# Performance work log

Measured on AMD Instinct MI355X. Metric: run time of the kernel, lower is better.

Reference implementation:

```python
import jax, jax.numpy as jnp
import numpy as np

THRESH = 0.7  # similarity_threshold from __init__
EPS = 1e-8    # torch cosine_similarity eps


def setup_inputs() -> dict:
    key = jax.random.key(0)
    ks = jax.random.split(key, 7)
    B, D, F, H, M, NMEM = 65536, 512, 10, 512, 256, 1024
    return {
        "query_features": jax.random.normal(ks[0], (B, D), jnp.float32),
        "B_mat": jax.random.normal(ks[1], (D, F), jnp.float32),
        "W1": jax.random.normal(ks[2], (2 * F, H), jnp.float32) * 0.05,
        "b1": jax.random.normal(ks[3], (H,), jnp.float32) * 0.01,
        "W2": jax.random.normal(ks[4], (H, M), jnp.float32) * 0.05,
        "b2": jax.random.normal(ks[5], (M,), jnp.float32) * 0.01,
        "memory_bank": jax.random.normal(ks[6], (NMEM, M), jnp.float32),
    }


def reference(query_features, B_mat, W1, b1, W2, b2, memory_bank):
    # Fourier features (eq. 8): [B, 2F]
    xp = query_features @ B_mat
    ff = jnp.concatenate([jnp.sin(xp), jnp.cos(xp)], axis=-1)
    # memory_net MLP -> query vectors [B, M]
    h = jax.nn.relu(ff @ W1 + b1)
    q = h @ W2 + b2
    # cosine similarity q vs memory bank (torch semantics: dot / max(|a||b|, eps))
    qn = jnp.linalg.norm(q, axis=-1, keepdims=True)          # [B,1]
    mn = jnp.linalg.norm(memory_bank, axis=-1, keepdims=True)  # [N,1]
    sim = (q @ memory_bank.T) / jnp.maximum(qn * mn.T, EPS)   # [B,N]
    max_sim = jnp.max(sim, axis=1)                            # [B]
    max_idx = jnp.argmax(sim, axis=1)                         # [B]
    relevant = memory_bank[max_idx]                           # [B,M] gather
    relevant = jnp.where((max_sim < THRESH)[:, None], 0.0, relevant)
    return relevant
```

## Files before the change

kernel.cpp:

```cpp
#include <hip/hip_runtime.h>
#include <hip/hip_bf16.h>


typedef __attribute__((ext_vector_type(8))) short short8;
typedef __attribute__((ext_vector_type(4))) float f32x4;

#define MFMA(a, b, c) __builtin_amdgcn_mfma_f32_16x16x32_bf16((a), (b), (c), 0, 0, 0)

static __device__ __forceinline__ short bfb(float f) {
  return (short)__builtin_bit_cast(unsigned short, __float2bfloat16(f));
}
static __device__ __forceinline__ unsigned short bf16bits(float f) {
  return __builtin_bit_cast(unsigned short, __float2bfloat16(f));
}
static __device__ __forceinline__ float sel10(const float a[10], int i) {
  float v = a[0];
#pragma unroll
  for (int j = 1; j < 10; ++j) v = (i == j) ? a[j] : v;
  return v;
}

typedef const __attribute__((address_space(1))) unsigned int* gas_p;
typedef __attribute__((address_space(3))) unsigned int* las_p;
static __device__ __forceinline__ void async16(const void* g, void* l) {
  __builtin_amdgcn_global_load_lds((gas_p)g, (las_p)l, 16, 0, 0);
}

__global__ __launch_bounds__(256) void prep_ff_kernel(
    const float* __restrict__ W1, const float* __restrict__ W2,
    const float* __restrict__ mem, const float* __restrict__ query,
    const float* __restrict__ Bmat, __hip_bfloat16* __restrict__ W1p,
    __hip_bfloat16* __restrict__ W2p, __hip_bfloat16* __restrict__ Mp,
    __hip_bfloat16* __restrict__ ff) {
  __shared__ __align__(16) float Bl[10 * 512];
  const int b = blockIdx.x, tid = threadIdx.x;
  if (b < 16) {
    float* invl = Bl;
    const int w = tid >> 6, lane = tid & 63, g = lane >> 4, jj = lane & 15;
    {
      int r = w * 16 + jj;
      const float4* m4 = (const float4*)(mem + (size_t)(b * 64 + r) * 256);
      float ss = 0.f;
      for (int t = 0; t < 16; ++t) {
        float4 v = m4[g * 16 + t];
        ss += v.x * v.x + v.y * v.y + v.z * v.z + v.w * v.w;
      }
      ss += __shfl_xor(ss, 16);
      ss += __shfl_xor(ss, 32);
      if (g == 0) invl[r] = rsqrtf(fmaxf(ss, 1e-30f));
    }
    __syncthreads();
    for (int u = 0; u < 64; ++u) {
      int t = u * 256 + tid;
      int j = t & 7, lane2 = (t >> 3) & 63, kt = (t >> 9) & 7, nl = t >> 12;
      int g2 = lane2 >> 4, jp = lane2 & 15;
      int nloc = nl * 16 + jp;
      int kap = 32 * kt + 16 * (j >> 2) + 4 * g2 + (j & 3);
      float v = mem[(size_t)(b * 64 + nloc) * 256 + kap] * invl[nloc];
      Mp[(size_t)b * 16384 + t] = __float2bfloat16(v);
    }
  } else if (b == 16) {
    for (int idx = tid; idx < 16384; idx += 256) {
      int j = idx & 7, lane2 = (idx >> 3) & 63, ct = idx >> 9;
      int g2 = lane2 >> 4, jp = lane2 & 15;
      int k = 8 * g2 + j;
      float v = (k < 20) ? W1[k * 512 + ct * 16 + jp] : 0.f;
      W1p[idx] = __float2bfloat16(v);
    }
  } else if (b < 33) {
    int bb = b - 17;
    for (int u = 0; u < 32; ++u) {
      int idx = bb * 8192 + u * 256 + tid;
      int j = idx & 7, lane2 = (idx >> 3) & 63, c = (idx >> 9) & 15, kt = idx >> 13;
      int g2 = lane2 >> 4, jp = lane2 & 15;
      int kap = 32 * kt + 16 * (j >> 2) + 4 * g2 + (j & 3);
      W2p[idx] = __float2bfloat16(W2[(size_t)kap * 256 + c * 16 + jp]);
    }
  } else {
    const int bb = b - 33;
    for (int i = tid; i < 5120; i += 256) {
      int d = i / 10, f = i - d * 10;
      Bl[f * 512 + d] = Bmat[i];
    }
    __syncthreads();
    const int wv = tid >> 6, lane = tid & 63;
    const int g = lane >> 4, jj = lane & 15;
    const long r0 = (long)bb * 32 + (wv * 4 + g) * 2;
    const float4* qa = (const float4*)(query + r0 * 512);
    const float4* qb = (const float4*)(query + (r0 + 1) * 512);

    float acc[2][10];
#pragma unroll
    for (int f = 0; f < 10; ++f) { acc[0][f] = 0.f; acc[1][f] = 0.f; }
#pragma unroll
    for (int k = 0; k < 8; ++k) {
      float4 va = qa[jj + 16 * k];
      float4 vb = qb[jj + 16 * k];
#pragma unroll
      for (int f = 0; f < 10; ++f) {
        float4 bv = *(const float4*)(Bl + f * 512 + 4 * (jj + 16 * k));
        acc[0][f] = fmaf(va.x, bv.x, fmaf(va.y, bv.y, fmaf(va.z, bv.z, fmaf(va.w, bv.w, acc[0][f]))));
        acc[1][f] = fmaf(vb.x, bv.x, fmaf(vb.y, bv.y, fmaf(vb.z, bv.z, fmaf(vb.w, bv.w, acc[1][f]))));
      }
    }
#pragma unroll
    for (int r = 0; r < 2; ++r) {
#pragma unroll
      for (int f = 0; f < 10; ++f) {
        float s = acc[r][f];
        s += __shfl_xor(s, 1); s += __shfl_xor(s, 2);
        s += __shfl_xor(s, 4); s += __shfl_xor(s, 8);
        acc[r][f] = s;
      }
      int base = (jj < 5) ? 2 * jj : 2 * jj - 10;
      float a0 = sel10(acc[r], base);
      float a1 = sel10(acc[r], base + 1);
      float v0 = 0.f, v1 = 0.f;
      if (jj < 5) { v0 = sinf(a0); v1 = sinf(a1); }
      else if (jj < 10) { v0 = cosf(a0); v1 = cosf(a1); }
      ushort2 pk;
      pk.x = bf16bits(v0);
      pk.y = bf16bits(v1);
      ((ushort2*)ff)[(r0 + r) * 16 + jj] = pk;
    }
  }
}

#define STAGE_W2(slab, bufi)                                      \
  do {                                                            \
    const char* s_ = (const char*)W2p + (slab)*16384 + tid * 16;  \
    char* d_ = lds + (bufi)*16384 + tid * 16;                     \
    async16(s_, d_);                                              \
    async16(s_ + 4096, d_ + 4096);                                \
    async16(s_ + 8192, d_ + 8192);                                \
    async16(s_ + 12288, d_ + 12288);                              \
  } while (0)

#define STAGE_MP(slab, bufi)                                      \
  do {                                                            \
    const char* s_ = (const char*)Mp + (slab)*16384 + tid * 16;   \
    char* d_ = lds + 32768 + (bufi)*16384 + tid * 16;             \
    async16(s_, d_);                                              \
    async16(s_ + 4096, d_ + 4096);                                \
    async16(s_ + 8192, d_ + 8192);                                \
    async16(s_ + 12288, d_ + 12288);                              \
  } while (0)

__global__ __launch_bounds__(256, 2) void mega_kernel(
    const __hip_bfloat16* __restrict__ ff, const __hip_bfloat16* __restrict__ W1p,
    const float* __restrict__ b1, const __hip_bfloat16* __restrict__ W2p,
    const float* __restrict__ b2, const __hip_bfloat16* __restrict__ Mp,
    const float* __restrict__ mem, float* __restrict__ out) {
  __shared__ __align__(16) char lds[65536];
  const int tid = threadIdx.x, w = tid >> 6, lane = tid & 63;
  const int g = lane >> 4, jj = lane & 15;
  const int rowBase = blockIdx.x * 128 + w * 32;
  const f32x4 z4 = {0.f, 0.f, 0.f, 0.f};
  const short8* w1f = (const short8*)W1p;

  STAGE_W2(0, 0);

  short8 ffq[2];
#pragma unroll
  for (int rt = 0; rt < 2; ++rt)
    ffq[rt] = *(const short8*)(ff + (size_t)(rowBase + rt * 16 + jj) * 32 + g * 8);

  f32x4 acc3[2][16];
#pragma unroll
  for (int rt = 0; rt < 2; ++rt)
#pragma unroll
    for (int c = 0; c < 16; ++c) acc3[rt][c] = z4;

  short8 w1c0 = w1f[lane], w1c1 = w1f[64 + lane];

  __syncthreads();

  for (int t = 0; t < 16; ++t) {
    if (t < 15) STAGE_W2(t + 1, (t + 1) & 1);
    else STAGE_MP(0, 0);
    short8 w1n0 = w1c0, w1n1 = w1c1;
    if (t < 15) {
      w1n0 = w1f[(2 * t + 2) * 64 + lane];
      w1n1 = w1f[(2 * t + 3) * 64 + lane];
    }
    const char* buf = lds + (t & 1) * 16384;
    short8 hf[2];
#pragma unroll
    for (int half = 0; half < 2; ++half) {
      const int ct = 2 * t + half;
      f32x4 bb = *(const f32x4*)(b1 + ct * 16 + 4 * g);
      short8 a = half ? w1c1 : w1c0;
#pragma unroll
      for (int rt = 0; rt < 2; ++rt) {
        f32x4 d = MFMA(a, ffq[rt], z4);
#pragma unroll
        for (int i = 0; i < 4; ++i) {
          float v = d[i] + bb[i];
          v = v > 0.f ? v : 0.f;
          hf[rt][half * 4 + i] = bfb(v);
        }
      }
    }
#pragma unroll
    for (int c = 0; c < 16; ++c) {
      short8 bfr = *(const short8*)(buf + c * 1024 + lane * 16);
#pragma unroll
      for (int rt = 0; rt < 2; ++rt)
        acc3[rt][c] = MFMA(bfr, hf[rt], acc3[rt][c]);
    }
    w1c0 = w1n0;
    w1c1 = w1n1;
    __syncthreads();
  }

  short8 qfrag[2][8];
  float invqn[2];
#pragma unroll
  for (int rt = 0; rt < 2; ++rt) {
    float qn = 0.f;
#pragma unroll
    for (int c = 0; c < 16; ++c) {
      f32x4 bb = *(const f32x4*)(b2 + c * 16 + 4 * g);
#pragma unroll
      for (int i = 0; i < 4; ++i) {
        float v = acc3[rt][c][i] + bb[i];
        qn += v * v;
        qfrag[rt][c >> 1][(c & 1) * 4 + i] = bfb(v);
      }
    }
    qn += __shfl_xor(qn, 16);
    qn += __shfl_xor(qn, 32);
    invqn[rt] = rsqrtf(fmaxf(qn, 1e-30f));
  }

  float runmax[2][4];
  int runidx[2][4];
#pragma unroll
  for (int rt = 0; rt < 2; ++rt)
#pragma unroll
    for (int i = 0; i < 4; ++i) { runmax[rt][i] = -1e30f; runidx[rt][i] = 0; }

  for (int t = 0; t < 32; ++t) {
    if (t < 31) STAGE_MP(t + 1, (t + 1) & 1);
    const char* buf = lds + 32768 + (t & 1) * 16384;
    f32x4 a4[2][2];
#pragma unroll
    for (int rt = 0; rt < 2; ++rt)
#pragma unroll
      for (int nl = 0; nl < 2; ++nl) a4[rt][nl] = z4;
#pragma unroll
    for (int kt = 0; kt < 8; ++kt) {
#pragma unroll
      for (int nl = 0; nl < 2; ++nl) {
        short8 bfr = *(const short8*)(buf + (nl * 8 + kt) * 1024 + lane * 16);
#pragma unroll
        for (int rt = 0; rt < 2; ++rt)
          a4[rt][nl] = MFMA(qfrag[rt][kt], bfr, a4[rt][nl]);
      }
    }
#pragma unroll
    for (int nl = 0; nl < 2; ++nl) {
      int n = (t * 2 + nl) * 16 + jj;
#pragma unroll
      for (int rt = 0; rt < 2; ++rt)
#pragma unroll
        for (int i = 0; i < 4; ++i) {
          if (a4[rt][nl][i] > runmax[rt][i]) {
            runmax[rt][i] = a4[rt][nl][i];
            runidx[rt][i] = n;
          }
        }
    }
    __syncthreads();
  }

  const float4* mem4 = (const float4*)mem;
  float4* out4 = (float4*)out;
#pragma unroll
  for (int rt = 0; rt < 2; ++rt) {
#pragma unroll
    for (int i = 0; i < 4; ++i) {
#pragma unroll
      for (int o = 1; o < 16; o <<= 1) {
        float v2 = __shfl_xor(runmax[rt][i], o);
        int i2 = __shfl_xor(runidx[rt][i], o);
        if (v2 > runmax[rt][i] || (v2 == runmax[rt][i] && i2 < runidx[rt][i])) {
          runmax[rt][i] = v2;
          runidx[rt][i] = i2;
        }
      }
    }
#pragma unroll
    for (int i = 0; i < 4; ++i) {
      float iq = __shfl(invqn[rt], 4 * g + i, 64);
      float ms = runmax[rt][i] * iq;
      int s = (ms < 0.7f) ? -1 : runidx[rt][i];
      size_t row = (size_t)rowBase + rt * 16 + 4 * g + i;
#pragma unroll
      for (int cq = 0; cq < 4; ++cq) {
        int col = cq * 16 + jj;
        float4 v = {0.f, 0.f, 0.f, 0.f};
        if (s >= 0) v = mem4[(size_t)s * 64 + col];
        out4[row * 64 + col] = v;
      }
    }
  }
}

extern "C" void kernel_launch(void* const* d_in, const int* in_sizes, int n_in,
                              void* d_out, int out_size, void* d_ws, size_t ws_size,
                              hipStream_t stream) {
  const float* query = (const float*)d_in[0];
  const float* Bmat = (const float*)d_in[1];
  const float* W1 = (const float*)d_in[2];
  const float* b1 = (const float*)d_in[3];
  const float* W2 = (const float*)d_in[4];
  const float* b2 = (const float*)d_in[5];
  const float* mem = (const float*)d_in[6];
  float* out = (float*)d_out;

  char* ws = (char*)d_ws;
  __hip_bfloat16* ff = (__hip_bfloat16*)ws;
  __hip_bfloat16* Mp = (__hip_bfloat16*)(ws + 4194304);
  __hip_bfloat16* W2p = (__hip_bfloat16*)(ws + 4194304 + 524288);
  __hip_bfloat16* W1p = (__hip_bfloat16*)(ws + 4194304 + 786432);

  prep_ff_kernel<<<dim3(2081), dim3(256), 0, stream>>>(W1, W2, mem, query, Bmat,
                                                       W1p, W2p, Mp, ff);
  mega_kernel<<<dim3(512), dim3(256), 0, stream>>>(ff, W1p, b1, W2p, b2, Mp, mem, out);
}
```

Baseline: 101.0 us.

## Unify W2 and memory-bank staging into a triple-buffered 8KB slab pipeline

```diff
diff --git a/kernel.cpp b/kernel.cpp
--- a/kernel.cpp
+++ b/kernel.cpp
@@ -27,11 +27,11 @@
 }
 
 __global__ __launch_bounds__(256) void prep_ff_kernel(
-    const float* __restrict__ W1, const float* __restrict__ W2,
-    const float* __restrict__ mem, const float* __restrict__ query,
-    const float* __restrict__ Bmat, __hip_bfloat16* __restrict__ W1p,
-    __hip_bfloat16* __restrict__ W2p, __hip_bfloat16* __restrict__ Mp,
-    __hip_bfloat16* __restrict__ ff) {
+    const float* __restrict__ W1, const float* __restrict__ b1,
+    const float* __restrict__ W2, const float* __restrict__ mem,
+    const float* __restrict__ query, const float* __restrict__ Bmat,
+    __hip_bfloat16* __restrict__ W1p, __hip_bfloat16* __restrict__ W2p,
+    __hip_bfloat16* __restrict__ Mp, __hip_bfloat16* __restrict__ ff) {
   __shared__ __align__(16) float Bl[10 * 512];
   const int b = blockIdx.x, tid = threadIdx.x;
   if (b < 16) {
@@ -64,7 +64,9 @@
       int j = idx & 7, lane2 = (idx >> 3) & 63, ct = idx >> 9;
       int g2 = lane2 >> 4, jp = lane2 & 15;
       int k = 8 * g2 + j;
-      float v = (k < 20) ? W1[k * 512 + ct * 16 + jp] : 0.f;
+      float v = 0.f;
+      if (k < 20) v = W1[k * 512 + ct * 16 + jp];
+      else if (k == 20) v = b1[ct * 16 + jp];
       W1p[idx] = __float2bfloat16(v);
     }
   } else if (b < 33) {
@@ -118,6 +120,7 @@
       float v0 = 0.f, v1 = 0.f;
       if (jj < 5) { v0 = sinf(a0); v1 = sinf(a1); }
       else if (jj < 10) { v0 = cosf(a0); v1 = cosf(a1); }
+      else if (jj == 10) { v0 = 1.0f; }
       ushort2 pk;
       pk.x = bf16bits(v0);
       pk.y = bf16bits(v1);
@@ -126,113 +129,44 @@
   }
 }
 
-#define STAGE_W2(slab, bufi)                                      \
-  do {                                                            \
-    const char* s_ = (const char*)W2p + (slab)*16384 + tid * 16;  \
-    char* d_ = lds + (bufi)*16384 + tid * 16;                     \
-    async16(s_, d_);                                              \
-    async16(s_ + 4096, d_ + 4096);                                \
-    async16(s_ + 8192, d_ + 8192);                                \
-    async16(s_ + 12288, d_ + 12288);                              \
-  } while (0)
-
-#define STAGE_MP(slab, bufi)                                      \
-  do {                                                            \
-    const char* s_ = (const char*)Mp + (slab)*16384 + tid * 16;   \
-    char* d_ = lds + 32768 + (bufi)*16384 + tid * 16;             \
-    async16(s_, d_);                                              \
-    async16(s_ + 4096, d_ + 4096);                                \
-    async16(s_ + 8192, d_ + 8192);                                \
-    async16(s_ + 12288, d_ + 12288);                              \
+#define STAGE_SLAB(s)                                                       \
+  do {                                                                      \
+    const char* s_ = ((s) < 32 ? (const char*)W2p + (size_t)(s) * 8192      \
+                               : (const char*)Mp + (size_t)((s) - 32) * 8192); \
+    char* d_ = lds + 33792 + ((s) % 3) * 8192;                              \
+    async16(s_ + tid * 16, d_ + tid * 16);                                  \
+    async16(s_ + 4096 + tid * 16, d_ + 4096 + tid * 16);                    \
   } while (0)
 
 __global__ __launch_bounds__(256, 2) void mega_kernel(
     const __hip_bfloat16* __restrict__ ff, const __hip_bfloat16* __restrict__ W1p,
-    const float* __restrict__ b1, const __hip_bfloat16* __restrict__ W2p,
-    const float* __restrict__ b2, const __hip_bfloat16* __restrict__ Mp,
-    const float* __restrict__ mem, float* __restrict__ out) {
-  __shared__ __align__(16) char lds[65536];
+    const __hip_bfloat16* __restrict__ W2p, const float* __restrict__ b2,
+    const __hip_bfloat16* __restrict__ Mp, const float* __restrict__ mem,
+    float* __restrict__ out) {
+  __shared__ __align__(16) char lds[58368];
   const int tid = threadIdx.x, w = tid >> 6, lane = tid & 63;
   const int g = lane >> 4, jj = lane & 15;
   const int rowBase = blockIdx.x * 128 + w * 32;
   const f32x4 z4 = {0.f, 0.f, 0.f, 0.f};
-  const short8* w1f = (const short8*)W1p;
-
-  STAGE_W2(0, 0);
-
-  short8 ffq[2];
-#pragma unroll
-  for (int rt = 0; rt < 2; ++rt)
-    ffq[rt] = *(const short8*)(ff + (size_t)(rowBase + rt * 16 + jj) * 32 + g * 8);
+
+  short8 ffq0 = *(const short8*)(ff + (size_t)(rowBase + jj) * 32 + g * 8);
+  short8 ffq1 = *(const short8*)(ff + (size_t)(rowBase + 16 + jj) * 32 + g * 8);
+  {
+    float v = b2[tid];
+    *(float*)(lds + 32768 + tid * 4) = v;
+  }
+#pragma unroll
+  for (int r = 0; r < 8; ++r)
+    async16((const char*)W1p + r * 4096 + tid * 16, lds + r * 4096 + tid * 16);
+  STAGE_SLAB(0);
+  STAGE_SLAB(1);
 
   f32x4 acc3[2][16];
 #pragma unroll
-  for (int rt = 0; rt < 2; ++rt)
-#pragma unroll
-    for (int c = 0; c < 16; ++c) acc3[rt][c] = z4;
-
-  short8 w1c0 = w1f[lane], w1c1 = w1f[64 + lane];
-
-  __syncthreads();
-
-  for (int t = 0; t < 16; ++t) {
-    if (t < 15) STAGE_W2(t + 1, (t + 1) & 1);
-    else STAGE_MP(0, 0);
-    short8 w1n0 = w1c0, w1n1 = w1c1;
-    if (t < 15) {
-      w1n0 = w1f[(2 * t + 2) * 64 + lane];
-      w1n1 = w1f[(2 * t + 3) * 64 + lane];
-    }
-    const char* buf = lds + (t & 1) * 16384;
-    short8 hf[2];
-#pragma unroll
-    for (int half = 0; half < 2; ++half) {
-      const int ct = 2 * t + half;
-      f32x4 bb = *(const f32x4*)(b1 + ct * 16 + 4 * g);
-      short8 a = half ? w1c1 : w1c0;
-#pragma unroll
-      for (int rt = 0; rt < 2; ++rt) {
-        f32x4 d = MFMA(a, ffq[rt], z4);
-#pragma unroll
-        for (int i = 0; i < 4; ++i) {
-          float v = d[i] + bb[i];
-          v = v > 0.f ? v : 0.f;
-          hf[rt][half * 4 + i] = bfb(v);
-        }
-      }
-    }
-#pragma unroll
-    for (int c = 0; c < 16; ++c) {
-      short8 bfr = *(const short8*)(buf + c * 1024 + lane * 16);
-#pragma unroll
-      for (int rt = 0; rt < 2; ++rt)
-        acc3[rt][c] = MFMA(bfr, hf[rt], acc3[rt][c]);
-    }
-    w1c0 = w1n0;
-    w1c1 = w1n1;
-    __syncthreads();
-  }
-
+  for (int c = 0; c < 16; ++c) { acc3[0][c] = z4; acc3[1][c] = z4; }
+  short8 hf0, hf1;
   short8 qfrag[2][8];
   float invqn[2];
-#pragma unroll
-  for (int rt = 0; rt < 2; ++rt) {
-    float qn = 0.f;
-#pragma unroll
-    for (int c = 0; c < 16; ++c) {
-      f32x4 bb = *(const f32x4*)(b2 + c * 16 + 4 * g);
-#pragma unroll
-      for (int i = 0; i < 4; ++i) {
-        float v = acc3[rt][c][i] + bb[i];
-        qn += v * v;
-        qfrag[rt][c >> 1][(c & 1) * 4 + i] = bfb(v);
-      }
-    }
-    qn += __shfl_xor(qn, 16);
-    qn += __shfl_xor(qn, 32);
-    invqn[rt] = rsqrtf(fmaxf(qn, 1e-30f));
-  }
-
   float runmax[2][4];
   int runidx[2][4];
 #pragma unroll
@@ -240,38 +174,83 @@
 #pragma unroll
     for (int i = 0; i < 4; ++i) { runmax[rt][i] = -1e30f; runidx[rt][i] = 0; }
 
-  for (int t = 0; t < 32; ++t) {
-    if (t < 31) STAGE_MP(t + 1, (t + 1) & 1);
-    const char* buf = lds + 32768 + (t & 1) * 16384;
-    f32x4 a4[2][2];
-#pragma unroll
-    for (int rt = 0; rt < 2; ++rt)
-#pragma unroll
-      for (int nl = 0; nl < 2; ++nl) a4[rt][nl] = z4;
-#pragma unroll
-    for (int kt = 0; kt < 8; ++kt) {
-#pragma unroll
-      for (int nl = 0; nl < 2; ++nl) {
-        short8 bfr = *(const short8*)(buf + (nl * 8 + kt) * 1024 + lane * 16);
-#pragma unroll
-        for (int rt = 0; rt < 2; ++rt)
-          a4[rt][nl] = MFMA(qfrag[rt][kt], bfr, a4[rt][nl]);
-      }
-    }
-#pragma unroll
-    for (int nl = 0; nl < 2; ++nl) {
-      int n = (t * 2 + nl) * 16 + jj;
-#pragma unroll
-      for (int rt = 0; rt < 2; ++rt)
+  for (int t = 0; t < 96; ++t) {
+    if (t < 95) {
+      asm volatile("s_waitcnt vmcnt(2)" ::: "memory");
+    } else {
+      asm volatile("s_waitcnt vmcnt(0)" ::: "memory");
+    }
+    __builtin_amdgcn_s_barrier();
+    asm volatile("" ::: "memory");
+    __builtin_amdgcn_sched_barrier(0);
+    if (t + 2 < 96) STAGE_SLAB(t + 2);
+    const char* buf = lds + 33792 + (t % 3) * 8192;
+
+    if (t < 32) {
+      const int kt = t >> 1;
+      if ((t & 1) == 0) {
+        short8 a0 = *(const short8*)(lds + (2 * kt) * 1024 + lane * 16);
+        short8 a1 = *(const short8*)(lds + (2 * kt + 1) * 1024 + lane * 16);
+        f32x4 d00 = MFMA(a0, ffq0, z4);
+        f32x4 d01 = MFMA(a1, ffq0, z4);
+        f32x4 d10 = MFMA(a0, ffq1, z4);
+        f32x4 d11 = MFMA(a1, ffq1, z4);
 #pragma unroll
         for (int i = 0; i < 4; ++i) {
-          if (a4[rt][nl][i] > runmax[rt][i]) {
-            runmax[rt][i] = a4[rt][nl][i];
-            runidx[rt][i] = n;
+          hf0[i] = bfb(d00[i] > 0.f ? d00[i] : 0.f);
+          hf0[4 + i] = bfb(d01[i] > 0.f ? d01[i] : 0.f);
+          hf1[i] = bfb(d10[i] > 0.f ? d10[i] : 0.f);
+          hf1[4 + i] = bfb(d11[i] > 0.f ? d11[i] : 0.f);
+        }
+#pragma unroll
+        for (int c = 0; c < 8; ++c) {
+          short8 bfr = *(const short8*)(buf + c * 1024 + lane * 16);
+          acc3[0][c] = MFMA(bfr, hf0, acc3[0][c]);
+          acc3[1][c] = MFMA(bfr, hf1, acc3[1][c]);
+        }
+      } else {
+#pragma unroll
+        for (int c = 0; c < 8; ++c) {
+          short8 bfr = *(const short8*)(buf + c * 1024 + lane * 16);
+          acc3[0][8 + c] = MFMA(bfr, hf0, acc3[0][8 + c]);
+          acc3[1][8 + c] = MFMA(bfr, hf1, acc3[1][8 + c]);
+        }
+      }
+      if (t == 31) {
+        const float* b2l = (const float*)(lds + 32768);
+#pragma unroll
+        for (int rt = 0; rt < 2; ++rt) {
+          float qn = 0.f;
+#pragma unroll
+          for (int c = 0; c < 16; ++c) {
+            f32x4 bb = *(const f32x4*)(b2l + c * 16 + 4 * g);
+#pragma unroll
+            for (int i = 0; i < 4; ++i) {
+              float v = (rt ? acc3[1][c][i] : acc3[0][c][i]) + bb[i];
+              qn += v * v;
+              qfrag[rt][c >> 1][(c & 1) * 4 + i] = bfb(v);
+            }
           }
-        }
-    }
-    __syncthreads();
+          qn += __shfl_xor(qn, 16);
+          qn += __shfl_xor(qn, 32);
+          invqn[rt] = rsqrtf(fmaxf(qn, 1e-30f));
+        }
+      }
+    } else {
+      f32x4 a40 = z4, a41 = z4;
+#pragma unroll
+      for (int kt = 0; kt < 8; ++kt) {
+        short8 bfr = *(const short8*)(buf + kt * 1024 + lane * 16);
+        a40 = MFMA(qfrag[0][kt], bfr, a40);
+        a41 = MFMA(qfrag[1][kt], bfr, a41);
+      }
+      const int n = (t - 32) * 16 + jj;
+#pragma unroll
+      for (int i = 0; i < 4; ++i) {
+        if (a40[i] > runmax[0][i]) { runmax[0][i] = a40[i]; runidx[0][i] = n; }
+        if (a41[i] > runmax[1][i]) { runmax[1][i] = a41[i]; runidx[1][i] = n; }
+      }
+    }
   }
 
   const float4* mem4 = (const float4*)mem;
@@ -325,7 +304,7 @@
   __hip_bfloat16* W2p = (__hip_bfloat16*)(ws + 4194304 + 524288);
   __hip_bfloat16* W1p = (__hip_bfloat16*)(ws + 4194304 + 786432);
 
-  prep_ff_kernel<<<dim3(2081), dim3(256), 0, stream>>>(W1, W2, mem, query, Bmat,
-                                                       W1p, W2p, Mp, ff);
-  mega_kernel<<<dim3(512), dim3(256), 0, stream>>>(ff, W1p, b1, W2p, b2, Mp, mem, out);
-}
+  prep_ff_kernel<<<dim3(2081), dim3(256), 0, stream>>>(W1, b1, W2, mem, query,
+                                                       Bmat, W1p, W2p, Mp, ff);
+  mega_kernel<<<dim3(512), dim3(256), 0, stream>>>(ff, W1p, W2p, b2, Mp, mem, out);
+}
```

Measured after the change: 175.2 us. 73.4% more time.
